# Kernel optimization log

Hardware: AMD Instinct MI355X
Metric: run time of the kernel (lower is better)

The kernel has to match this reference:

```python
import jax, jax.numpy as jnp
import numpy as np

HEADS = 8
NUM_LANDMARKS = 256
PINV_ITERS = 6
KERNEL = 33
PAD = KERNEL // 2


def moore_penrose_iter_pinv(x, iters=PINV_ITERS):
    abs_x = jnp.abs(x)
    col = abs_x.sum(axis=-1)
    row = abs_x.sum(axis=-2)
    z = jnp.swapaxes(x, -1, -2) / (jnp.max(col) * jnp.max(row))
    I = jnp.eye(x.shape[-1], dtype=x.dtype)
    for _ in range(iters):
        xz = x @ z
        z = 0.25 * z @ (13.0 * I - xz @ (15.0 * I - xz @ (7.0 * I - xz)))
    return z


def setup_inputs() -> dict:
    key = jax.random.key(0)
    k1, k2, k3, k4 = jax.random.split(key, 4)
    b, h, n, d = 2, HEADS, 8192, 64
    q = jax.random.normal(k1, (b, h, n, d), dtype=jnp.float32)
    k = jax.random.normal(k2, (b, h, n, d), dtype=jnp.float32)
    v = jax.random.normal(k3, (b, h, n, d), dtype=jnp.float32)
    conv_w = jax.random.normal(k4, (HEADS, 1, KERNEL, 1), dtype=jnp.float32) * 0.05
    return {"q": q, "k": k, "v": v, "conv_w": conv_w}


def reference(q, k, v, conv_w):
    b, h, n, d = q.shape
    m = NUM_LANDMARKS
    l = n // m  # n chosen divisible by m, so no padding branch

    # landmarks: mean over contiguous groups of size l
    q_land = q.reshape(b, h, m, l, d).sum(axis=-2) / l  # [b,h,m,d]
    k_land = k.reshape(b, h, m, l, d).sum(axis=-2) / l

    sim1 = jnp.einsum('bhid,bhjd->bhij', q, k_land)       # [b,h,n,m]
    sim2 = jnp.einsum('bhid,bhjd->bhij', q_land, k_land)  # [b,h,m,m]
    sim3 = jnp.einsum('bhid,bhjd->bhij', q_land, k)       # [b,h,m,n]

    attn1 = jax.nn.softmax(sim1, axis=-1)
    attn2 = jax.nn.softmax(sim2, axis=-1)
    attn3 = jax.nn.softmax(sim3, axis=-1)

    attn2_inv = moore_penrose_iter_pinv(attn2, PINV_ITERS)

    out = attn1 @ (attn2_inv @ (attn3 @ v))  # [b,h,n,d]

    # depthwise residual conv over sequence dim (Conv2d(h,h,(33,1),groups=h,bias=False) on v)
    res = jax.lax.conv_general_dilated(
        v, conv_w,
        window_strides=(1, 1),
        padding=((PAD, PAD), (0, 0)),
        dimension_numbers=('NCHW', 'OIHW', 'NCHW'),
        feature_group_count=HEADS,
    )
    return out + res
```

## Files before the change

kernel.cpp:

```cpp
#include <hip/hip_runtime.h>


#define N_SEQ 8192
#define NBH   16
#define MLAND 256
#define DHEAD 64
#define NSPLIT3 8

typedef __attribute__((ext_vector_type(8))) short bfrag;
typedef __attribute__((ext_vector_type(8))) _Float16 hfrag;
typedef __attribute__((ext_vector_type(4))) float f32x4;

__device__ __forceinline__ void fma8(float (&o)[8], float p, const float4& a, const float4& b) {
    o[0] += p * a.x; o[1] += p * a.y; o[2] += p * a.z; o[3] += p * a.w;
    o[4] += p * b.x; o[5] += p * b.y; o[6] += p * b.z; o[7] += p * b.w;
}

__device__ __forceinline__ unsigned short f2bf(float f) {
    unsigned u = __float_as_uint(f);
    unsigned r = u + 0x7fffu + ((u >> 16) & 1u);
    return (unsigned short)(r >> 16);
}
__device__ __forceinline__ float bf2f(unsigned short h) {
    return __uint_as_float(((unsigned)h) << 16);
}

__device__ __forceinline__ void splitbf(float v, unsigned short& h, unsigned short& l) {
    unsigned bits = __float_as_uint(v);
    h = (unsigned short)(bits >> 16);
    float r = v - __uint_as_float(bits & 0xffff0000u);
    l = (unsigned short)(__float_as_uint(r) >> 16);
}

__device__ __forceinline__ void splith(float v, unsigned short& h, unsigned short& l) {
    _Float16 hf = (_Float16)v;
    _Float16 lf = (_Float16)(v - (float)hf);
    h = __builtin_bit_cast(unsigned short, hf);
    l = __builtin_bit_cast(unsigned short, lf);
}

__device__ __forceinline__ void stage16(const float* __restrict__ src,
                                        unsigned short* dh, unsigned short* dl) {
    unsigned* ph = (unsigned*)dh;
    unsigned* pl = (unsigned*)dl;
    #pragma unroll
    for (int o = 0; o < 16; o += 4) {
        float4 a = *(const float4*)(src + o);
        float vv[4] = {a.x, a.y, a.z, a.w};
        unsigned short h[4], l[4];
        #pragma unroll
        for (int u = 0; u < 4; ++u) splitbf(vv[u], h[u], l[u]);
        ph[o / 2]     = (unsigned)h[0] | ((unsigned)h[1] << 16);
        ph[o / 2 + 1] = (unsigned)h[2] | ((unsigned)h[3] << 16);
        pl[o / 2]     = (unsigned)l[0] | ((unsigned)l[1] << 16);
        pl[o / 2 + 1] = (unsigned)l[2] | ((unsigned)l[3] << 16);
    }
}

__device__ __forceinline__ void stageh16(const float* __restrict__ src,
                                         unsigned short* dh, unsigned short* dl) {
    unsigned* ph = (unsigned*)dh;
    unsigned* pl = (unsigned*)dl;
    #pragma unroll
    for (int o = 0; o < 16; o += 4) {
        float4 a = *(const float4*)(src + o);
        float vv[4] = {a.x, a.y, a.z, a.w};
        unsigned short h[4], l[4];
        #pragma unroll
        for (int u = 0; u < 4; ++u) splith(vv[u], h[u], l[u]);
        ph[o / 2]     = (unsigned)h[0] | ((unsigned)h[1] << 16);
        ph[o / 2 + 1] = (unsigned)h[2] | ((unsigned)h[3] << 16);
        pl[o / 2]     = (unsigned)l[0] | ((unsigned)l[1] << 16);
        pl[o / 2 + 1] = (unsigned)l[2] | ((unsigned)l[3] << 16);
    }
}

__global__ __launch_bounds__(64) void k_landmarks(
    const float* __restrict__ q, const float* __restrict__ k,
    float* __restrict__ ql, float* __restrict__ kl)
{
    int mi = blockIdx.x & 255;
    int bh = blockIdx.x >> 8;
    const float* src = blockIdx.y ? k : q;
    float*       dst = blockIdx.y ? kl : ql;
    int t = threadIdx.x;
    const float* s = src + ((size_t)bh * N_SEQ + (size_t)mi * 32) * DHEAD;
    float acc = 0.f;
    #pragma unroll
    for (int j = 0; j < 32; ++j) acc += s[j * DHEAD + t];
    dst[((size_t)bh * MLAND + mi) * DHEAD + t] = acc * (1.f / 32.f);
}

__global__ __launch_bounds__(256) void k_sim2_softmax(
    const float* __restrict__ ql, const float* __restrict__ kl,
    float* __restrict__ attn2)
{
    int bh = blockIdx.x >> 8;
    int i  = blockIdx.x & 255;
    int t  = threadIdx.x;
    __shared__ float qrow[DHEAD];
    __shared__ float wred[8];
    if (t < DHEAD) qrow[t] = ql[((size_t)bh * MLAND + i) * DHEAD + t];
    __syncthreads();
    const float* krow = kl + ((size_t)bh * MLAND + t) * DHEAD;
    float s = 0.f;
    #pragma unroll
    for (int kk = 0; kk < DHEAD; kk += 4) {
        float4 k4 = *(const float4*)(krow + kk);
        s += qrow[kk] * k4.x + qrow[kk + 1] * k4.y + qrow[kk + 2] * k4.z + qrow[kk + 3] * k4.w;
    }
    float m = s;
    #pragma unroll
    for (int o = 32; o > 0; o >>= 1) m = fmaxf(m, __shfl_xor(m, o, 64));
    int wave = t >> 6, lane = t & 63;
    if (lane == 0) wred[wave] = m;
    __syncthreads();
    float bm = fmaxf(fmaxf(wred[0], wred[1]), fmaxf(wred[2], wred[3]));
    float e = __expf(s - bm);
    float sum = e;
    #pragma unroll
    for (int o = 32; o > 0; o >>= 1) sum += __shfl_xor(sum, o, 64);
    if (lane == 0) wred[4 + wave] = sum;
    __syncthreads();
    float bs = wred[4] + wred[5] + wred[6] + wred[7];
    attn2[((size_t)bh * MLAND + i) * MLAND + t] = e / bs;
}

__global__ __launch_bounds__(256) void k_scale_reduce(
    const float* __restrict__ x, float* __restrict__ scl)
{
    int bh = blockIdx.x, t = threadIdx.x;
    const float* xb = x + (size_t)bh * MLAND * MLAND;
    float colsum = 0.f, rowsum = 0.f;
    for (int i = 0; i < MLAND; ++i) colsum += xb[(size_t)i * MLAND + t];
    for (int j = 0; j < MLAND; ++j) rowsum += xb[(size_t)t * MLAND + j];
    __shared__ float red[256];
    red[t] = rowsum;
    __syncthreads();
    for (int o = 128; o > 0; o >>= 1) {
        if (t < o) red[t] = fmaxf(red[t], red[t + o]);
        __syncthreads();
    }
    if (t == 0) atomicMax((unsigned int*)&scl[0], __float_as_uint(red[0]));
    __syncthreads();
    red[t] = colsum;
    __syncthreads();
    for (int o = 128; o > 0; o >>= 1) {
        if (t < o) red[t] = fmaxf(red[t], red[t + o]);
        __syncthreads();
    }
    if (t == 0) atomicMax((unsigned int*)&scl[1], __float_as_uint(red[0]));
}

__global__ __launch_bounds__(256) void k_zinit(
    const float* __restrict__ x, float* __restrict__ z,
    const float* __restrict__ scl)
{
    __shared__ float tile[32][33];
    int bh = blockIdx.z;
    int i0 = blockIdx.y * 32, j0 = blockIdx.x * 32;
    int t = threadIdx.x;
    int lx = t & 31, ly = t >> 5;
    const float* xb = x + (size_t)bh * MLAND * MLAND;
    float*       zb = z + (size_t)bh * MLAND * MLAND;
    #pragma unroll
    for (int p = 0; p < 4; ++p)
        tile[ly + 8 * p][lx] = xb[(size_t)(i0 + ly + 8 * p) * MLAND + j0 + lx];
    __syncthreads();
    float inv = 1.0f / (scl[0] * scl[1]);
    #pragma unroll
    for (int p = 0; p < 4; ++p)
        zb[(size_t)(j0 + ly + 8 * p) * MLAND + i0 + lx] = tile[lx][ly + 8 * p] * inv;
}

__global__ __launch_bounds__(256) void k_bmm_mfma(
    const float* __restrict__ A, const float* __restrict__ B, float* __restrict__ C,
    int N, float diag, float bscale, float outscale)
{
    __shared__ unsigned short sm[4 * 64 * 72];
    unsigned short* Ah = sm;
    unsigned short* Al = sm + 64 * 72;
    unsigned short* Bh = sm + 2 * 64 * 72;
    unsigned short* Bl = sm + 3 * 64 * 72;

    int bh = blockIdx.z;
    const float* Ab = A + (size_t)bh * 65536;
    const float* Bb = B + (size_t)bh * 256 * N;
    float*       Cb = C + (size_t)bh * 256 * N;
    int m0 = blockIdx.y * 64, n0 = blockIdx.x * 64;
    int t = threadIdx.x;
    int wave = t >> 6, lane = t & 63;
    int l15 = lane & 15, quad = lane >> 4;

    f32x4 acc[4] = {};

    for (int kc = 0; kc < 256; kc += 64) {
        __syncthreads();
        {
            int m = t & 63, ks = (t >> 6) * 16;
            const float* src = Ab + (size_t)(m0 + m) * 256 + kc + ks;
            unsigned short h[16], l[16];
            #pragma unroll
            for (int o = 0; o < 16; o += 4) {
                float4 a = *(const float4*)(src + o);
                float vv[4] = {a.x, a.y, a.z, a.w};
                #pragma unroll
                for (int u = 0; u < 4; ++u) {
                    h[o + u] = f2bf(vv[u]);
                    l[o + u] = f2bf(vv[u] - bf2f(h[o + u]));
                }
            }
            unsigned* dh = (unsigned*)&Ah[m * 72 + ks];
            unsigned* dl = (unsigned*)&Al[m * 72 + ks];
            #pragma unroll
            for (int o = 0; o < 8; ++o) {
                dh[o] = (unsigned)h[2 * o] | ((unsigned)h[2 * o + 1] << 16);
                dl[o] = (unsigned)l[2 * o] | ((unsigned)l[2 * o + 1] << 16);
            }
        }
        {
            int kk = t & 63, ns = (t >> 6) * 16;
            int gk = kc + kk;
            const float* src = Bb + (size_t)gk * N + n0 + ns;
            #pragma unroll
            for (int o = 0; o < 16; o += 4) {
                float4 bv = *(const float4*)(src + o);
                float vv[4] = {bv.x, bv.y, bv.z, bv.w};
                #pragma unroll
                for (int u = 0; u < 4; ++u) {
                    float val = bscale * vv[u];
                    if (gk == n0 + ns + o + u) val += diag;
                    unsigned short hh = f2bf(val);
                    Bh[(ns + o + u) * 72 + kk] = hh;
                    Bl[(ns + o + u) * 72 + kk] = f2bf(val - bf2f(hh));
                }
            }
        }
        __syncthreads();

        #pragma unroll
        for (int k0 = 0; k0 < 64; k0 += 32) {
            int kf = k0 + quad * 8;
            int am = wave * 16 + l15;
            bfrag ah = *(const bfrag*)&Ah[am * 72 + kf];
            bfrag al = *(const bfrag*)&Al[am * 72 + kf];
            #pragma unroll
            for (int j = 0; j < 4; ++j) {
                int bn = j * 16 + l15;
                bfrag bhf = *(const bfrag*)&Bh[bn * 72 + kf];
                bfrag blf = *(const bfrag*)&Bl[bn * 72 + kf];
                acc[j] = __builtin_amdgcn_mfma_f32_16x16x32_bf16(al, bhf, acc[j], 0, 0, 0);
                acc[j] = __builtin_amdgcn_mfma_f32_16x16x32_bf16(ah, blf, acc[j], 0, 0, 0);
                acc[j] = __builtin_amdgcn_mfma_f32_16x16x32_bf16(ah, bhf, acc[j], 0, 0, 0);
            }
        }
    }

    #pragma unroll
    for (int j = 0; j < 4; ++j) {
        #pragma unroll
        for (int r = 0; r < 4; ++r) {
            int row = m0 + wave * 16 + quad * 4 + r;
            Cb[(size_t)row * N + n0 + j * 16 + l15] = acc[j][r] * outscale;
        }
    }
}

__global__ __launch_bounds__(256, 2) void k_attn3_partial(
    const float* __restrict__ ql, const float* __restrict__ k,
    const float* __restrict__ v, float* __restrict__ pO,
    float* __restrict__ pm, float* __restrict__ pl)
{
    __shared__ __align__(16) unsigned short sm3[36864];
    unsigned short* QH = sm3;
    unsigned short* QL = sm3 + 4608;
    unsigned short* KH = sm3 + 9216;
    unsigned short* KL = sm3 + 13824;
    unsigned short* VH = sm3 + 18432;
    unsigned short* VL = sm3 + 23040;
    unsigned short* PH = sm3 + 27648;
    unsigned short* PL = sm3 + 32256;

    int sp = blockIdx.x;
    int m0 = blockIdx.y * 64;
    int bh = blockIdx.z;
    int t = threadIdx.x;
    int wave = t >> 6, lane = t & 63;
    int l15 = lane & 15, quad = lane >> 4;

    {
        int row = t & 63, ds = (t >> 6) * 16;
        const float* src = ql + ((size_t)bh * MLAND + m0 + row) * DHEAD + ds;
        stage16(src, &QH[row * 72 + ds], &QL[row * 72 + ds]);
    }
    __syncthreads();

    bfrag aqh[2], aql[2];
    #pragma unroll
    for (int ks = 0; ks < 2; ++ks) {
        aqh[ks] = *(const bfrag*)&QH[(wave * 16 + l15) * 72 + ks * 32 + quad * 8];
        aql[ks] = *(const bfrag*)&QL[(wave * 16 + l15) * 72 + ks * 32 + quad * 8];
    }

    f32x4 O[4] = {};
    float M[4], L[4];
    #pragma unroll
    for (int r = 0; r < 4; ++r) { M[r] = -1e30f; L[r] = 0.f; }

    const float* kb = k + (size_t)bh * N_SEQ * DHEAD;
    const float* vb = v + (size_t)bh * N_SEQ * DHEAD;

    for (int cc = 0; cc < 16; ++cc) {
        int c0 = sp * 1024 + cc * 64;
        __syncthreads();
        {
            int key = t & 63, ds = (t >> 6) * 16;
            stage16(kb + (size_t)(c0 + key) * DHEAD + ds,
                    &KH[key * 72 + ds], &KL[key * 72 + ds]);
        }
        {
            int key = t & 63, dq = (t >> 6) * 16;
            const float* src = vb + (size_t)(c0 + key) * DHEAD + dq;
            #pragma unroll
            for (int o = 0; o < 16; o += 4) {
                float4 a = *(const float4*)(src + o);
                float vv[4] = {a.x, a.y, a.z, a.w};
                #pragma unroll
                for (int u = 0; u < 4; ++u) {
                    unsigned short h, l;
                    splitbf(vv[u], h, l);
                    VH[(dq + o + u) * 72 + key] = h;
                    VL[(dq + o + u) * 72 + key] = l;
                }
            }
        }
        __syncthreads();

        f32x4 S4[4] = {};
        __builtin_amdgcn_s_setprio(1);
        #pragma unroll
        for (int ks = 0; ks < 2; ++ks) {
            #pragma unroll
            for (int ni = 0; ni < 4; ++ni) {
                bfrag bkh = *(const bfrag*)&KH[(ni * 16 + l15) * 72 + ks * 32 + quad * 8];
                bfrag bkl = *(const bfrag*)&KL[(ni * 16 + l15) * 72 + ks * 32 + quad * 8];
                S4[ni] = __builtin_amdgcn_mfma_f32_16x16x32_bf16(aql[ks], bkh, S4[ni], 0, 0, 0);
                S4[ni] = __builtin_amdgcn_mfma_f32_16x16x32_bf16(aqh[ks], bkl, S4[ni], 0, 0, 0);
                S4[ni] = __builtin_amdgcn_mfma_f32_16x16x32_bf16(aqh[ks], bkh, S4[ni], 0, 0, 0);
            }
        }
        __builtin_amdgcn_s_setprio(0);

        #pragma unroll
        for (int r = 0; r < 4; ++r) {
            float mv = fmaxf(fmaxf(S4[0][r], S4[1][r]), fmaxf(S4[2][r], S4[3][r]));
            mv = fmaxf(mv, __shfl_xor(mv, 1, 16));
            mv = fmaxf(mv, __shfl_xor(mv, 2, 16));
            mv = fmaxf(mv, __shfl_xor(mv, 4, 16));
            mv = fmaxf(mv, __shfl_xor(mv, 8, 16));
            float nM = fmaxf(M[r], mv);
            float alpha = __expf(M[r] - nM);
            M[r] = nM;
            float rs = 0.f;
            #pragma unroll
            for (int ni = 0; ni < 4; ++ni) {
                float p = __expf(S4[ni][r] - nM);
                S4[ni][r] = p;
                rs += p;
            }
            rs += __shfl_xor(rs, 1, 16);
            rs += __shfl_xor(rs, 2, 16);
            rs += __shfl_xor(rs, 4, 16);
            rs += __shfl_xor(rs, 8, 16);
            L[r] = L[r] * alpha + rs;
            #pragma unroll
            for (int ni = 0; ni < 4; ++ni) O[ni][r] *= alpha;
        }

        #pragma unroll
        for (int ni = 0; ni < 4; ++ni) {
            #pragma unroll
            for (int r = 0; r < 4; ++r) {
                int row = wave * 16 + quad * 4 + r;
                int col = ni * 16 + l15;
                unsigned short h, l;
                splitbf(S4[ni][r], h, l);
                PH[row * 72 + col] = h;
                PL[row * 72 + col] = l;
            }
        }

        __builtin_amdgcn_s_setprio(1);
        #pragma unroll
        for (int ks = 0; ks < 2; ++ks) {
            bfrag aph = *(const bfrag*)&PH[(wave * 16 + l15) * 72 + ks * 32 + quad * 8];
            bfrag apl = *(const bfrag*)&PL[(wave * 16 + l15) * 72 + ks * 32 + quad * 8];
            #pragma unroll
            for (int ni = 0; ni < 4; ++ni) {
                bfrag bvh = *(const bfrag*)&VH[(ni * 16 + l15) * 72 + ks * 32 + quad * 8];
                bfrag bvl = *(const bfrag*)&VL[(ni * 16 + l15) * 72 + ks * 32 + quad * 8];
                O[ni] = __builtin_amdgcn_mfma_f32_16x16x32_bf16(apl, bvh, O[ni], 0, 0, 0);
                O[ni] = __builtin_amdgcn_mfma_f32_16x16x32_bf16(aph, bvl, O[ni], 0, 0, 0);
                O[ni] = __builtin_amdgcn_mfma_f32_16x16x32_bf16(aph, bvh, O[ni], 0, 0, 0);
            }
        }
        __builtin_amdgcn_s_setprio(0);
    }

    int base = (bh * NSPLIT3 + sp) * MLAND + m0;
    #pragma unroll
    for (int r = 0; r < 4; ++r) {
        int row = wave * 16 + quad * 4 + r;
        if (l15 == 0) { pm[base + row] = M[r]; pl[base + row] = L[r]; }
        #pragma unroll
        for (int ni = 0; ni < 4; ++ni)
            pO[(size_t)(base + row) * DHEAD + ni * 16 + l15] = O[ni][r];
    }
}

__global__ __launch_bounds__(64) void k_attn3_combine(
    const float* __restrict__ pO, const float* __restrict__ pm,
    const float* __restrict__ pl, float* __restrict__ kv)
{
    int bh = blockIdx.x >> 8;
    int m  = blockIdx.x & 255;
    int d  = threadIdx.x;
    float M = -1e30f;
    #pragma unroll
    for (int s = 0; s < NSPLIT3; ++s) M = fmaxf(M, pm[(bh * NSPLIT3 + s) * MLAND + m]);
    float L = 0.f, O = 0.f;
    #pragma unroll
    for (int s = 0; s < NSPLIT3; ++s) {
        int base = (bh * NSPLIT3 + s) * MLAND + m;
        float w = __expf(pm[base] - M);
        L += pl[base] * w;
        O += w * pO[(size_t)base * DHEAD + d];
    }
    kv[((size_t)bh * MLAND + m) * DHEAD + d] = O / L;
}

__global__ __launch_bounds__(256, 2) void k_attn1_mfma(
    const float* __restrict__ q, const float* __restrict__ kl,
    const float* __restrict__ W, float* __restrict__ out)
{
    __shared__ __align__(16) unsigned short sm1[36864];
    unsigned short* QH = sm1;
    unsigned short* QL = sm1 + 4608;
    unsigned short* KH = sm1 + 9216;
    unsigned short* KL = sm1 + 13824;
    unsigned short* WH = sm1 + 18432;
    unsigned short* WL = sm1 + 23040;
    unsigned short* PH = sm1 + 27648;
    unsigned short* PL = sm1 + 32256;

    int bh = blockIdx.y;
    int r0 = blockIdx.x * 64;
    int t = threadIdx.x;
    int wave = t >> 6, lane = t & 63;
    int l15 = lane & 15, quad = lane >> 4;

    {
        int row = t & 63, ds = (t >> 6) * 16;
        const float* src = q + ((size_t)bh * N_SEQ + r0 + row) * DHEAD + ds;
        stageh16(src, &QH[row * 72 + ds], &QL[row * 72 + ds]);
    }
    __syncthreads();

    hfrag aqh[2], aql[2];
    #pragma unroll
    for (int ks = 0; ks < 2; ++ks) {
        aqh[ks] = *(const hfrag*)&QH[(wave * 16 + l15) * 72 + ks * 32 + quad * 8];
        aql[ks] = *(const hfrag*)&QL[(wave * 16 + l15) * 72 + ks * 32 + quad * 8];
    }

    f32x4 O4[4] = {};
    float M[4], L[4];
    #pragma unroll
    for (int r = 0; r < 4; ++r) { M[r] = -1e30f; L[r] = 0.f; }

    for (int mc = 0; mc < 4; ++mc) {
        __syncthreads();
        {
            int key = t & 63, ds = (t >> 6) * 16;
            stageh16(kl + ((size_t)bh * MLAND + mc * 64 + key) * DHEAD + ds,
                     &KH[key * 72 + ds], &KL[key * 72 + ds]);
        }
        {
            int key = t & 63, dq = (t >> 6) * 16;
            const float* src = W + ((size_t)bh * MLAND + mc * 64 + key) * DHEAD + dq;
            #pragma unroll
            for (int o = 0; o < 16; o += 4) {
                float4 a = *(const float4*)(src + o);
                float vv[4] = {a.x * 0.015625f, a.y * 0.015625f,
                               a.z * 0.015625f, a.w * 0.015625f};
                #pragma unroll
                for (int u = 0; u < 4; ++u) {
                    unsigned short h, l;
                    splith(vv[u], h, l);
                    WH[(dq + o + u) * 72 + key] = h;
                    WL[(dq + o + u) * 72 + key] = l;
                }
            }
        }
        __syncthreads();

        f32x4 S4[4] = {};
        __builtin_amdgcn_s_setprio(1);
        #pragma unroll
        for (int ks = 0; ks < 2; ++ks) {
            #pragma unroll
            for (int ni = 0; ni < 4; ++ni) {
                hfrag bkh = *(const hfrag*)&KH[(ni * 16 + l15) * 72 + ks * 32 + quad * 8];
                hfrag bkl = *(const hfrag*)&KL[(ni * 16 + l15) * 72 + ks * 32 + quad * 8];
                S4[ni] = __builtin_amdgcn_mfma_f32_16x16x32_f16(aql[ks], bkh, S4[ni], 0, 0, 0);
                S4[ni] = __builtin_amdgcn_mfma_f32_16x16x32_f16(aqh[ks], bkl, S4[ni], 0, 0, 0);
                S4[ni] = __builtin_amdgcn_mfma_f32_16x16x32_f16(aqh[ks], bkh, S4[ni], 0, 0, 0);
            }
        }
        __builtin_amdgcn_s_setprio(0);

        #pragma unroll
        for (int r = 0; r < 4; ++r) {
            float mv = fmaxf(fmaxf(S4[0][r], S4[1][r]), fmaxf(S4[2][r], S4[3][r]));
            mv = fmaxf(mv, __shfl_xor(mv, 1, 16));
            mv = fmaxf(mv, __shfl_xor(mv, 2, 16));
            mv = fmaxf(mv, __shfl_xor(mv, 4, 16));
            mv = fmaxf(mv, __shfl_xor(mv, 8, 16));
            float nM = fmaxf(M[r], mv);
            float alpha = __expf(M[r] - nM);
            M[r] = nM;
            float rs = 0.f;
            #pragma unroll
            for (int ni = 0; ni < 4; ++ni) {
                float p = __expf(S4[ni][r] - nM);
                S4[ni][r] = p;
                rs += p;
            }
            rs += __shfl_xor(rs, 1, 16);
            rs += __shfl_xor(rs, 2, 16);
            rs += __shfl_xor(rs, 4, 16);
            rs += __shfl_xor(rs, 8, 16);
            L[r] = L[r] * alpha + rs;
            #pragma unroll
            for (int ni = 0; ni < 4; ++ni) O4[ni][r] *= alpha;
        }

        #pragma unroll
        for (int ni = 0; ni < 4; ++ni) {
            #pragma unroll
            for (int r = 0; r < 4; ++r) {
                int row = wave * 16 + quad * 4 + r;
                int col = ni * 16 + l15;
                unsigned short h, l;
                splith(S4[ni][r], h, l);
                PH[row * 72 + col] = h;
                PL[row * 72 + col] = l;
            }
        }

        __builtin_amdgcn_s_setprio(1);
        #pragma unroll
        for (int ks = 0; ks < 2; ++ks) {
            hfrag aph = *(const hfrag*)&PH[(wave * 16 + l15) * 72 + ks * 32 + quad * 8];
            hfrag apl = *(const hfrag*)&PL[(wave * 16 + l15) * 72 + ks * 32 + quad * 8];
            #pragma unroll
            for (int ni = 0; ni < 4; ++ni) {
                hfrag bwh = *(const hfrag*)&WH[(ni * 16 + l15) * 72 + ks * 32 + quad * 8];
                hfrag bwl = *(const hfrag*)&WL[(ni * 16 + l15) * 72 + ks * 32 + quad * 8];
                O4[ni] = __builtin_amdgcn_mfma_f32_16x16x32_f16(apl, bwh, O4[ni], 0, 0, 0);
                O4[ni] = __builtin_amdgcn_mfma_f32_16x16x32_f16(aph, bwl, O4[ni], 0, 0, 0);
                O4[ni] = __builtin_amdgcn_mfma_f32_16x16x32_f16(aph, bwh, O4[ni], 0, 0, 0);
            }
        }
        __builtin_amdgcn_s_setprio(0);
    }

    float inv[4];
    #pragma unroll
    for (int r = 0; r < 4; ++r) inv[r] = 64.0f / L[r];
    #pragma unroll
    for (int r = 0; r < 4; ++r) {
        int row = wave * 16 + quad * 4 + r;
        float* dst = out + ((size_t)bh * N_SEQ + r0 + row) * DHEAD;
        #pragma unroll
        for (int ni = 0; ni < 4; ++ni)
            dst[ni * 16 + l15] = O4[ni][r] * inv[r];
    }
}

__global__ __launch_bounds__(256) void k_conv_add(
    const float* __restrict__ v, const float* __restrict__ cw,
    float* __restrict__ out)
{
    __shared__ __align__(16) float smem[160 * 68];
    __shared__ float wgt[33];
    int bh = blockIdx.y;
    int r0 = blockIdx.x * 128;
    int t = threadIdx.x;
    int wave = t >> 6, lane = t & 63;
    int ly = lane >> 3, lx = lane & 7;
    int rb = wave * 32 + ly * 4;

    if (t < 33) wgt[t] = cw[(bh & 7) * 33 + t];

    for (int rr = t; rr < 160; rr += 256) {
        int gr = r0 - 16 + rr;
        bool ok = (gr >= 0) && (gr < N_SEQ);
        const float* src = v + ((size_t)bh * N_SEQ + gr) * DHEAD;
        #pragma unroll
        for (int c = 0; c < 64; c += 4) {
            float4 val = ok ? *(const float4*)(src + c) : make_float4(0.f, 0.f, 0.f, 0.f);
            *(float4*)&smem[rr * 68 + c] = val;
        }
    }
    __syncthreads();

    float res[4][8] = {};
    #pragma unroll
    for (int w = 0; w < 36; ++w) {
        float4 va  = *(const float4*)&smem[(rb + w) * 68 + lx * 8];
        float4 vb4 = *(const float4*)&smem[(rb + w) * 68 + lx * 8 + 4];
        #pragma unroll
        for (int i = 0; i < 4; ++i) {
            if (w - i >= 0 && w - i <= 32) {
                float wv = wgt[w - i];
                fma8(res[i], wv, va, vb4);
            }
        }
    }

    #pragma unroll
    for (int i = 0; i < 4; ++i) {
        float* dst = out + ((size_t)bh * N_SEQ + r0 + rb + i) * DHEAD + lx * 8;
        float4 o0 = *(const float4*)dst;
        float4 o1 = *(const float4*)(dst + 4);
        *(float4*)dst = make_float4(o0.x + res[i][0], o0.y + res[i][1],
                                    o0.z + res[i][2], o0.w + res[i][3]);
        *(float4*)(dst + 4) = make_float4(o1.x + res[i][4], o1.y + res[i][5],
                                          o1.z + res[i][6], o1.w + res[i][7]);
    }
}

extern "C" void kernel_launch(void* const* d_in, const int* in_sizes, int n_in,
                              void* d_out, int out_size, void* d_ws, size_t ws_size,
                              hipStream_t stream)
{
    (void)in_sizes; (void)n_in; (void)out_size; (void)ws_size;
    const float* q  = (const float*)d_in[0];
    const float* k  = (const float*)d_in[1];
    const float* v  = (const float*)d_in[2];
    const float* cw = (const float*)d_in[3];
    float* out = (float*)d_out;
    float* ws  = (float*)d_ws;

    const size_t LM = (size_t)NBH * MLAND * DHEAD;
    const size_t MM = (size_t)NBH * MLAND * MLAND;
    float* ql  = ws;
    float* kl  = ql  + LM;
    float* x   = kl  + LM;
    float* z   = x   + MM;
    float* z2  = z   + MM;
    float* xz  = z2  + MM;
    float* t2  = xz  + MM;
    float* t3  = t2  + MM;
    float* kv  = t3  + MM;
    float* W   = kv  + LM;
    float* scl = W   + LM;
    float* pm  = scl + 16;
    float* pl  = pm + (size_t)NBH * 16 * MLAND;

    float* pO = z2;

    hipMemsetAsync(scl, 0, 32, stream);

    k_landmarks<<<dim3(NBH * MLAND, 2), 64, 0, stream>>>(q, k, ql, kl);
    k_sim2_softmax<<<NBH * MLAND, 256, 0, stream>>>(ql, kl, x);
    k_scale_reduce<<<NBH, 256, 0, stream>>>(x, scl);
    k_zinit<<<dim3(8, 8, NBH), 256, 0, stream>>>(x, z, scl);

    k_attn3_partial<<<dim3(NSPLIT3, 4, NBH), 256, 0, stream>>>(ql, k, v, pO, pm, pl);
    k_attn3_combine<<<NBH * MLAND, 64, 0, stream>>>(pO, pm, pl, kv);

    float* zc = z;
    float* zn = z2;
    for (int it = 0; it < 6; ++it) {
        k_bmm_mfma<<<dim3(4, 4, NBH), 256, 0, stream>>>(x,  zc, xz, 256,  0.f,  1.f, 1.f);
        k_bmm_mfma<<<dim3(4, 4, NBH), 256, 0, stream>>>(xz, xz, t2, 256,  7.f, -1.f, 1.f);
        k_bmm_mfma<<<dim3(4, 4, NBH), 256, 0, stream>>>(xz, t2, t3, 256, 15.f, -1.f, 1.f);
        k_bmm_mfma<<<dim3(4, 4, NBH), 256, 0, stream>>>(zc, t3, zn, 256, 13.f, -1.f, 0.25f);
        float* tt = zc; zc = zn; zn = tt;
    }
    k_bmm_mfma<<<dim3(1, 4, NBH), 256, 0, stream>>>(zc, kv, W, 64, 0.f, 1.f, 1.f);

    k_attn1_mfma<<<dim3(128, NBH), 256, 0, stream>>>(q, kl, W, out);
    k_conv_add<<<dim3(64, NBH), 256, 0, stream>>>(v, cw, out);
}
```

Measured before the change: 645.2 us.

## Store pinv intermediates as pre-split bf16 hi/lo planes between matmuls

Intermediate matrices of the Newton-Schulz pseudo-inverse (x, z, xz, t2, t3, kv) are now stored as separate bf16 high and low planes instead of fp32. The matmul kernel loads these planes directly into shared memory instead of converting fp32 to split bf16 on every tile load, and writes its output already split. Negation is done by flipping sign bits, and only diagonal elements are re-split when the identity term is added. This is meant to cut per-load conversion ALU work in the 25 chained matmuls at the same memory footprint. The trade-off is truncation-based splitting (splitbf) instead of round-to-nearest, which may change accuracy slightly.

```diff
diff --git a/kernel.cpp b/kernel.cpp
--- a/kernel.cpp
+++ b/kernel.cpp
@@ -6,6 +6,8 @@
 #define MLAND 256
 #define DHEAD 64
 #define NSPLIT3 8
+#define MM_E  (NBH * MLAND * MLAND)
+#define LM_E  (NBH * MLAND * DHEAD)
 
 typedef __attribute__((ext_vector_type(8))) short bfrag;
 typedef __attribute__((ext_vector_type(8))) _Float16 hfrag;
@@ -16,11 +18,6 @@
     o[4] += p * b.x; o[5] += p * b.y; o[6] += p * b.z; o[7] += p * b.w;
 }
 
-__device__ __forceinline__ unsigned short f2bf(float f) {
-    unsigned u = __float_as_uint(f);
-    unsigned r = u + 0x7fffu + ((u >> 16) & 1u);
-    return (unsigned short)(r >> 16);
-}
 __device__ __forceinline__ float bf2f(unsigned short h) {
     return __uint_as_float(((unsigned)h) << 16);
 }
@@ -93,8 +90,10 @@
 
 __global__ __launch_bounds__(256) void k_sim2_softmax(
     const float* __restrict__ ql, const float* __restrict__ kl,
-    float* __restrict__ attn2)
-{
+    unsigned short* __restrict__ xs)
+{
+    unsigned short* xh = xs;
+    unsigned short* xl = xs + MM_E;
     int bh = blockIdx.x >> 8;
     int i  = blockIdx.x & 255;
     int t  = threadIdx.x;
@@ -123,17 +122,30 @@
     if (lane == 0) wred[4 + wave] = sum;
     __syncthreads();
     float bs = wred[4] + wred[5] + wred[6] + wred[7];
-    attn2[((size_t)bh * MLAND + i) * MLAND + t] = e / bs;
+    float val = e / bs;
+    unsigned short h, l;
+    splitbf(val, h, l);
+    size_t idx = ((size_t)bh * MLAND + i) * MLAND + t;
+    xh[idx] = h;
+    xl[idx] = l;
 }
 
 __global__ __launch_bounds__(256) void k_scale_reduce(
-    const float* __restrict__ x, float* __restrict__ scl)
-{
+    const unsigned short* __restrict__ xs, float* __restrict__ scl)
+{
+    const unsigned short* xh = xs;
+    const unsigned short* xl = xs + MM_E;
     int bh = blockIdx.x, t = threadIdx.x;
-    const float* xb = x + (size_t)bh * MLAND * MLAND;
+    size_t b = (size_t)bh * MLAND * MLAND;
     float colsum = 0.f, rowsum = 0.f;
-    for (int i = 0; i < MLAND; ++i) colsum += xb[(size_t)i * MLAND + t];
-    for (int j = 0; j < MLAND; ++j) rowsum += xb[(size_t)t * MLAND + j];
+    for (int i = 0; i < MLAND; ++i) {
+        size_t idx = b + (size_t)i * MLAND + t;
+        colsum += bf2f(xh[idx]) + bf2f(xl[idx]);
+    }
+    for (int j = 0; j < MLAND; ++j) {
+        size_t idx = b + (size_t)t * MLAND + j;
+        rowsum += bf2f(xh[idx]) + bf2f(xl[idx]);
+    }
     __shared__ float red[256];
     red[t] = rowsum;
     __syncthreads();
@@ -153,28 +165,42 @@
 }
 
 __global__ __launch_bounds__(256) void k_zinit(
-    const float* __restrict__ x, float* __restrict__ z,
+    const unsigned short* __restrict__ xs, unsigned short* __restrict__ zs,
     const float* __restrict__ scl)
 {
+    const unsigned short* xh = xs;
+    const unsigned short* xl = xs + MM_E;
+    unsigned short* zh = zs;
+    unsigned short* zl = zs + MM_E;
     __shared__ float tile[32][33];
     int bh = blockIdx.z;
     int i0 = blockIdx.y * 32, j0 = blockIdx.x * 32;
     int t = threadIdx.x;
     int lx = t & 31, ly = t >> 5;
-    const float* xb = x + (size_t)bh * MLAND * MLAND;
-    float*       zb = z + (size_t)bh * MLAND * MLAND;
-    #pragma unroll
-    for (int p = 0; p < 4; ++p)
-        tile[ly + 8 * p][lx] = xb[(size_t)(i0 + ly + 8 * p) * MLAND + j0 + lx];
+    size_t b = (size_t)bh * MLAND * MLAND;
+    #pragma unroll
+    for (int p = 0; p < 4; ++p) {
+        size_t idx = b + (size_t)(i0 + ly + 8 * p) * MLAND + j0 + lx;
+        tile[ly + 8 * p][lx] = bf2f(xh[idx]) + bf2f(xl[idx]);
+    }
     __syncthreads();
     float inv = 1.0f / (scl[0] * scl[1]);
     #pragma unroll
-    for (int p = 0; p < 4; ++p)
-        zb[(size_t)(j0 + ly + 8 * p) * MLAND + i0 + lx] = tile[lx][ly + 8 * p] * inv;
-}
-
-__global__ __launch_bounds__(256) void k_bmm_mfma(
-    const float* __restrict__ A, const float* __restrict__ B, float* __restrict__ C,
+    for (int p = 0; p < 4; ++p) {
+        float val = tile[lx][ly + 8 * p] * inv;
+        unsigned short h, l;
+        splitbf(val, h, l);
+        size_t idx = b + (size_t)(j0 + ly + 8 * p) * MLAND + i0 + lx;
+        zh[idx] = h;
+        zl[idx] = l;
+    }
+}
+
+__global__ __launch_bounds__(256) void k_bmm_planes(
+    const unsigned short* __restrict__ Ahp, const unsigned short* __restrict__ Alp,
+    const unsigned short* __restrict__ Bhp, const unsigned short* __restrict__ Blp,
+    unsigned short* __restrict__ Chp, unsigned short* __restrict__ Clp,
+    float* __restrict__ Cf,
     int N, float diag, float bscale, float outscale)
 {
     __shared__ unsigned short sm[4 * 64 * 72];
@@ -184,13 +210,13 @@
     unsigned short* Bl = sm + 3 * 64 * 72;
 
     int bh = blockIdx.z;
-    const float* Ab = A + (size_t)bh * 65536;
-    const float* Bb = B + (size_t)bh * 256 * N;
-    float*       Cb = C + (size_t)bh * 256 * N;
+    const size_t abase = (size_t)bh * 65536;
+    const size_t bbase = (size_t)bh * 256 * N;
     int m0 = blockIdx.y * 64, n0 = blockIdx.x * 64;
     int t = threadIdx.x;
     int wave = t >> 6, lane = t & 63;
     int l15 = lane & 15, quad = lane >> 4;
+    unsigned sflip = (bscale < 0.f) ? 0x8000u : 0u;
 
     f32x4 acc[4] = {};
 
@@ -198,42 +224,31 @@
         __syncthreads();
         {
             int m = t & 63, ks = (t >> 6) * 16;
-            const float* src = Ab + (size_t)(m0 + m) * 256 + kc + ks;
-            unsigned short h[16], l[16];
-            #pragma unroll
-            for (int o = 0; o < 16; o += 4) {
-                float4 a = *(const float4*)(src + o);
-                float vv[4] = {a.x, a.y, a.z, a.w};
-                #pragma unroll
-                for (int u = 0; u < 4; ++u) {
-                    h[o + u] = f2bf(vv[u]);
-                    l[o + u] = f2bf(vv[u] - bf2f(h[o + u]));
-                }
-            }
-            unsigned* dh = (unsigned*)&Ah[m * 72 + ks];
-            unsigned* dl = (unsigned*)&Al[m * 72 + ks];
-            #pragma unroll
-            for (int o = 0; o < 8; ++o) {
-                dh[o] = (unsigned)h[2 * o] | ((unsigned)h[2 * o + 1] << 16);
-                dl[o] = (unsigned)l[2 * o] | ((unsigned)l[2 * o + 1] << 16);
-            }
+            size_t off = abase + (size_t)(m0 + m) * 256 + kc + ks;
+            *(uint4*)&Ah[m * 72 + ks]     = *(const uint4*)&Ahp[off];
+            *(uint4*)&Ah[m * 72 + ks + 8] = *(const uint4*)&Ahp[off + 8];
+            *(uint4*)&Al[m * 72 + ks]     = *(const uint4*)&Alp[off];
+            *(uint4*)&Al[m * 72 + ks + 8] = *(const uint4*)&Alp[off + 8];
         }
         {
             int kk = t & 63, ns = (t >> 6) * 16;
             int gk = kc + kk;
-            const float* src = Bb + (size_t)gk * N + n0 + ns;
-            #pragma unroll
-            for (int o = 0; o < 16; o += 4) {
-                float4 bv = *(const float4*)(src + o);
-                float vv[4] = {bv.x, bv.y, bv.z, bv.w};
-                #pragma unroll
-                for (int u = 0; u < 4; ++u) {
-                    float val = bscale * vv[u];
-                    if (gk == n0 + ns + o + u) val += diag;
-                    unsigned short hh = f2bf(val);
-                    Bh[(ns + o + u) * 72 + kk] = hh;
-                    Bl[(ns + o + u) * 72 + kk] = f2bf(val - bf2f(hh));
+            size_t off = bbase + (size_t)gk * N + n0 + ns;
+            unsigned short hb[16], lb[16];
+            *(uint4*)&hb[0] = *(const uint4*)&Bhp[off];
+            *(uint4*)&hb[8] = *(const uint4*)&Bhp[off + 8];
+            *(uint4*)&lb[0] = *(const uint4*)&Blp[off];
+            *(uint4*)&lb[8] = *(const uint4*)&Blp[off + 8];
+            #pragma unroll
+            for (int u = 0; u < 16; ++u) {
+                unsigned short h = hb[u] ^ sflip;
+                unsigned short l = lb[u] ^ sflip;
+                if (diag != 0.f && gk == n0 + ns + u) {
+                    float val = diag + bf2f(h) + bf2f(l);
+                    splitbf(val, h, l);
                 }
+                Bh[(ns + u) * 72 + kk] = h;
+                Bl[(ns + u) * 72 + kk] = l;
             }
         }
         __syncthreads();
@@ -256,12 +271,29 @@
         }
     }
 
-    #pragma unroll
-    for (int j = 0; j < 4; ++j) {
-        #pragma unroll
-        for (int r = 0; r < 4; ++r) {
-            int row = m0 + wave * 16 + quad * 4 + r;
-            Cb[(size_t)row * N + n0 + j * 16 + l15] = acc[j][r] * outscale;
+    size_t cbase = (size_t)bh * 256 * N;
+    if (Cf) {
+        #pragma unroll
+        for (int j = 0; j < 4; ++j) {
+            #pragma unroll
+            for (int r = 0; r < 4; ++r) {
+                int row = m0 + wave * 16 + quad * 4 + r;
+                Cf[cbase + (size_t)row * N + n0 + j * 16 + l15] = acc[j][r] * outscale;
+            }
+        }
+    } else {
+        #pragma unroll
+        for (int j = 0; j < 4; ++j) {
+            #pragma unroll
+            for (int r = 0; r < 4; ++r) {
+                int row = m0 + wave * 16 + quad * 4 + r;
+                float val = acc[j][r] * outscale;
+                unsigned short h, l;
+                splitbf(val, h, l);
+                size_t idx = cbase + (size_t)row * N + n0 + j * 16 + l15;
+                Chp[idx] = h;
+                Clp[idx] = l;
+            }
         }
     }
 }
@@ -420,8 +452,10 @@
 
 __global__ __launch_bounds__(64) void k_attn3_combine(
     const float* __restrict__ pO, const float* __restrict__ pm,
-    const float* __restrict__ pl, float* __restrict__ kv)
-{
+    const float* __restrict__ pl, unsigned short* __restrict__ kvs)
+{
+    unsigned short* kvh = kvs;
+    unsigned short* kvl = kvs + LM_E;
     int bh = blockIdx.x >> 8;
     int m  = blockIdx.x & 255;
     int d  = threadIdx.x;
@@ -436,7 +470,12 @@
         L += pl[base] * w;
         O += w * pO[(size_t)base * DHEAD + d];
     }
-    kv[((size_t)bh * MLAND + m) * DHEAD + d] = O / L;
+    float val = O / L;
+    unsigned short h, l;
+    splitbf(val, h, l);
+    size_t idx = ((size_t)bh * MLAND + m) * DHEAD + d;
+    kvh[idx] = h;
+    kvl[idx] = l;
 }
 
 __global__ __launch_bounds__(256, 2) void k_attn1_mfma(
@@ -653,44 +692,67 @@
     float* out = (float*)d_out;
     float* ws  = (float*)d_ws;
 
-    const size_t LM = (size_t)NBH * MLAND * DHEAD;
-    const size_t MM = (size_t)NBH * MLAND * MLAND;
+    const size_t LM = (size_t)LM_E;
+    const size_t MM = (size_t)MM_E;
+
     float* ql  = ws;
     float* kl  = ql  + LM;
-    float* x   = kl  + LM;
-    float* z   = x   + MM;
-    float* z2  = z   + MM;
-    float* xz  = z2  + MM;
-    float* t2  = xz  + MM;
-    float* t3  = t2  + MM;
-    float* kv  = t3  + MM;
-    float* W   = kv  + LM;
+    float* xsf = kl  + LM;
+    float* zsf = xsf + MM;
+    float* big = zsf + MM;
+    float* kvf = big + 4 * MM;
+    float* W   = kvf + LM;
     float* scl = W   + LM;
     float* pm  = scl + 16;
-    float* pl  = pm + (size_t)NBH * 16 * MLAND;
-
-    float* pO = z2;
+    float* pl  = pm + (size_t)NBH * NSPLIT3 * MLAND;
+
+    float* pO = big;
+
+    unsigned short* xs  = (unsigned short*)xsf;
+    unsigned short* zs  = (unsigned short*)zsf;
+    unsigned short* bgu = (unsigned short*)big;
+    unsigned short* kvs = (unsigned short*)kvf;
+
+    unsigned short* zh  = zs;
+    unsigned short* zl  = zs + MM;
+    unsigned short* xh  = xs;
+    unsigned short* xl  = xs + MM;
+    unsigned short* z2h = bgu;
+    unsigned short* z2l = bgu + MM;
+    unsigned short* xzh = bgu + 2 * MM;
+    unsigned short* xzl = bgu + 3 * MM;
+    unsigned short* t2h = bgu + 4 * MM;
+    unsigned short* t2l = bgu + 5 * MM;
+    unsigned short* t3h = bgu + 6 * MM;
+    unsigned short* t3l = bgu + 7 * MM;
+    unsigned short* kvh = kvs;
+    unsigned short* kvl = kvs + LM;
 
     hipMemsetAsync(scl, 0, 32, stream);
 
     k_landmarks<<<dim3(NBH * MLAND, 2), 64, 0, stream>>>(q, k, ql, kl);
-    k_sim2_softmax<<<NBH * MLAND, 256, 0, stream>>>(ql, kl, x);
-    k_scale_reduce<<<NBH, 256, 0, stream>>>(x, scl);
-    k_zinit<<<dim3(8, 8, NBH), 256, 0, stream>>>(x, z, scl);
+    k_sim2_softmax<<<NBH * MLAND, 256, 0, stream>>>(ql, kl, xs);
+    k_scale_reduce<<<NBH, 256, 0, stream>>>(xs, scl);
+    k_zinit<<<dim3(8, 8, NBH), 256, 0, stream>>>(xs, zs, scl);
 
     k_attn3_partial<<<dim3(NSPLIT3, 4, NBH), 256, 0, stream>>>(ql, k, v, pO, pm, pl);
-    k_attn3_combine<<<NBH * MLAND, 64, 0, stream>>>(pO, pm, pl, kv);
-
-    float* zc = z;
-    float* zn = z2;
+    k_attn3_combine<<<NBH * MLAND, 64, 0, stream>>>(pO, pm, pl, kvs);
+
+    unsigned short *zch = zh, *zcl = zl, *znh = z2h, *znl = z2l;
     for (int it = 0; it < 6; ++it) {
-        k_bmm_mfma<<<dim3(4, 4, NBH), 256, 0, stream>>>(x,  zc, xz, 256,  0.f,  1.f, 1.f);
-        k_bmm_mfma<<<dim3(4, 4, NBH), 256, 0, stream>>>(xz, xz, t2, 256,  7.f, -1.f, 1.f);
-        k_bmm_mfma<<<dim3(4, 4, NBH), 256, 0, stream>>>(xz, t2, t3, 256, 15.f, -1.f, 1.f);
-        k_bmm_mfma<<<dim3(4, 4, NBH), 256, 0, stream>>>(zc, t3, zn, 256, 13.f, -1.f, 0.25f);
-        float* tt = zc; zc = zn; zn = tt;
-    }
-    k_bmm_mfma<<<dim3(1, 4, NBH), 256, 0, stream>>>(zc, kv, W, 64, 0.f, 1.f, 1.f);
+        k_bmm_planes<<<dim3(4, 4, NBH), 256, 0, stream>>>(
+            xh, xl, zch, zcl, xzh, xzl, nullptr, 256, 0.f, 1.f, 1.f);
+        k_bmm_planes<<<dim3(4, 4, NBH), 256, 0, stream>>>(
+            xzh, xzl, xzh, xzl, t2h, t2l, nullptr, 256, 7.f, -1.f, 1.f);
+        k_bmm_planes<<<dim3(4, 4, NBH), 256, 0, stream>>>(
+            xzh, xzl, t2h, t2l, t3h, t3l, nullptr, 256, 15.f, -1.f, 1.f);
+        k_bmm_planes<<<dim3(4, 4, NBH), 256, 0, stream>>>(
+            zch, zcl, t3h, t3l, znh, znl, nullptr, 256, 13.f, -1.f, 0.25f);
+        unsigned short* th = zch; zch = znh; znh = th;
+        unsigned short* tl = zcl; zcl = znl; znl = tl;
+    }
+    k_bmm_planes<<<dim3(1, 4, NBH), 256, 0, stream>>>(
+        zch, zcl, kvh, kvl, nullptr, nullptr, W, 64, 0.f, 1.f, 1.f);
 
     k_attn1_mfma<<<dim3(128, NBH), 256, 0, stream>>>(q, kl, W, out);
     k_conv_add<<<dim3(64, NBH), 256, 0, stream>>>(v, cw, out);
```

Measured after the change: 632.6 us. No clear change (-2.0%).
